# Optimization experiments

Hardware: AMD Instinct MI355X
Metric: run time of the kernel (lower is better)

The kernel has to match this reference:

```python
import jax, jax.numpy as jnp
import numpy as np

N_GRID = 65160   # 181*360 lat-lon grid nodes (= self.size)
N_MESH = 40962   # level-6 icosphere nodes
N_TOT = N_GRID + N_MESH
E = 521280
IN_CH = 96
HID = 256
OUT_CH = 96


def setup_inputs() -> dict:
    key = jax.random.key(0)
    ks = jax.random.split(key, 12)
    inp = {
        'x': jax.random.normal(ks[0], (1, IN_CH, N_MESH), jnp.float32),
        'x_res_grid': jax.random.normal(ks[1], (1, IN_CH, N_GRID), jnp.float32),
        'edge_index': jax.random.randint(ks[2], (2, E), 0, N_TOT, jnp.int64),
        # GCNConv 1 (in_ch -> 256), glorot-ish scale
        'W1': jax.random.normal(ks[3], (IN_CH, HID), jnp.float32) * (2.0 / (IN_CH + HID)) ** 0.5,
        'b1': jnp.zeros((HID,), jnp.float32),
        # GCNConv 2 (256 -> 256)
        'W2': jax.random.normal(ks[4], (HID, HID), jnp.float32) * (2.0 / (HID + HID)) ** 0.5,
        'b2': jnp.zeros((HID,), jnp.float32),
        # Lmodel2: Linear(256,256) -> Linear(256,out_ch), xavier_normal
        'Wl1': jax.random.normal(ks[5], (HID, HID), jnp.float32) * (2.0 / (HID + HID)) ** 0.5,
        'bl1': jnp.zeros((HID,), jnp.float32),
        'Wl2': jax.random.normal(ks[6], (HID, OUT_CH), jnp.float32) * (2.0 / (HID + OUT_CH)) ** 0.5,
        'bl2': jnp.zeros((OUT_CH,), jnp.float32),
    }
    return inp


def _gcn_norm(edge_index, n_nodes):
    # PyG gcn_norm with add_self_loops=True, edge_weight=1
    loop = jnp.arange(n_nodes, dtype=edge_index.dtype)
    src = jnp.concatenate([edge_index[0], loop])
    dst = jnp.concatenate([edge_index[1], loop])
    deg = jnp.zeros((n_nodes,), jnp.float32).at[dst].add(1.0)
    dinv = jnp.where(deg > 0, jax.lax.rsqrt(deg), 0.0)
    norm = dinv[src] * dinv[dst]  # [E+N]
    return src, dst, norm


def _gcn_conv(h, W, b, src, dst, norm):
    # h: [B, N, C] -> [B, N, H]; x' = D^-1/2 (A+I) D^-1/2 (h W) + b
    m = h @ W                                   # [B, N, H]
    msg = m[:, src, :] * norm[None, :, None]    # [B, E+N, H]
    agg = jnp.zeros(m.shape, m.dtype).at[:, dst].add(msg)
    return agg + b


def reference(x, x_res_grid, edge_index, W1, b1, W2, b2, Wl1, bl1, Wl2, bl2):
    nodes = jnp.concatenate([x_res_grid, x], axis=-1)  # [B, C, N]
    h = nodes.transpose(0, 2, 1)                       # [B, N, C]
    n = h.shape[1]
    src, dst, norm = _gcn_norm(edge_index, n)
    h = _gcn_conv(h, W1, b1, src, dst, norm)
    h = jax.nn.gelu(h, approximate=False)              # torch nn.GELU (exact erf)
    h = _gcn_conv(h, W2, b2, src, dst, norm)           # [B, N, 256]
    g = h[:, :N_GRID, :]                               # slice grid nodes
    out = (g @ Wl1 + bl1) @ Wl2 + bl2                  # [B, size, out_ch]
    return out.transpose(0, 2, 1)                      # [B, out_ch, size]
```

## Files before the change

### kernel.cpp

```cpp
#include <hip/hip_runtime.h>
#include <math.h>

#define N_GRID 65160
#define N_MESH 40962
#define N_TOT  106122
#define NE     521280
#define IN_CH  96
#define HID    256
#define OUT_CH 96

typedef __attribute__((ext_vector_type(8))) short bf16x8;
typedef __attribute__((ext_vector_type(4))) float f32x4;

__device__ __forceinline__ unsigned short f2bf(float f) {
  unsigned u = __float_as_uint(f);
  return (unsigned short)((u + 0x7FFFu + ((u >> 16) & 1u)) >> 16);
}
__device__ __forceinline__ float bf2f(unsigned short s) {
  return __uint_as_float(((unsigned)s) << 16);
}
__device__ __forceinline__ float4 ldbf4(const unsigned short* p) {
  ushort4 u = *(const ushort4*)p;
  return make_float4(bf2f(u.x), bf2f(u.y), bf2f(u.z), bf2f(u.w));
}

__global__ void k_concat_transpose(const float* __restrict__ xg, const float* __restrict__ xm,
                                   unsigned short* __restrict__ h) {
  __shared__ float tile[IN_CH][65];
  int base = blockIdx.x * 64;
  int t = threadIdx.x;
#pragma unroll
  for (int it = 0; it < 24; ++it) {
    int lin = t + it * 256;
    int c  = lin >> 6;
    int n0 = lin & 63;
    int n = base + n0;
    float v = 0.f;
    if (n < N_TOT) {
      v = (n < N_GRID) ? xg[(size_t)c * N_GRID + n]
                       : xm[(size_t)c * N_MESH + (n - N_GRID)];
    }
    tile[c][n0] = v;
  }
  __syncthreads();
#pragma unroll
  for (int it = 0; it < 24; ++it) {
    int lin = t + it * 256;
    int c  = lin % 96;
    int n0 = lin / 96;
    int n = base + n0;
    if (n < N_TOT) h[(size_t)n * IN_CH + c] = f2bf(tile[c][n0]);
  }
}

__global__ void k_transpose_out(const float* __restrict__ tb, float* __restrict__ out) {
  __shared__ float tile[IN_CH][65];
  int base = blockIdx.x * 64;
  int t = threadIdx.x;
#pragma unroll
  for (int it = 0; it < 24; ++it) {
    int lin = t + it * 256;
    int c  = lin % 96;
    int n0 = lin / 96;
    int n = base + n0;
    if (n < N_GRID) tile[c][n0] = tb[(size_t)n * 96 + c];
  }
  __syncthreads();
#pragma unroll
  for (int it = 0; it < 24; ++it) {
    int lin = t + it * 256;
    int c  = lin >> 6;
    int n0 = lin & 63;
    int n = base + n0;
    if (n < N_GRID) out[(size_t)c * N_GRID + n] = tile[c][n0];
  }
}

__global__ void k_zeroi(int* __restrict__ p, int n) {
  int i = blockIdx.x * 256 + threadIdx.x;
  if (i < n) p[i] = 0;
}
__global__ void k_seti(int* __restrict__ p, int v) { *p = v; }

__global__ void k_hist(const int* __restrict__ dst, int* __restrict__ deg) {
  int e = blockIdx.x * 256 + threadIdx.x;
  if (e < NE) atomicAdd(&deg[dst[e]], 1);
}

__global__ void k_blocksum(const int* __restrict__ deg, int* __restrict__ bsum, int n) {
  __shared__ int s[256];
  int i = blockIdx.x * 256 + threadIdx.x;
  s[threadIdx.x] = (i < n) ? deg[i] : 0;
  __syncthreads();
  for (int st = 128; st > 0; st >>= 1) {
    if (threadIdx.x < st) s[threadIdx.x] += s[threadIdx.x + st];
    __syncthreads();
  }
  if (threadIdx.x == 0) bsum[blockIdx.x] = s[0];
}

__global__ void k_scanbsum(int* __restrict__ bsum, int nb) {
  __shared__ int s[512];
  int t = threadIdx.x;
  int v = (t < nb) ? bsum[t] : 0;
  s[t] = v;
  __syncthreads();
  for (int off = 1; off < 512; off <<= 1) {
    int x = (t >= off) ? s[t - off] : 0;
    __syncthreads();
    s[t] += x;
    __syncthreads();
  }
  if (t < nb) bsum[t] = s[t] - v;
}

__global__ void k_offsets(const int* __restrict__ deg, const int* __restrict__ bsum,
                          int* __restrict__ off, int* __restrict__ cur, int n) {
  __shared__ int s[256];
  int i = blockIdx.x * 256 + threadIdx.x;
  int v = (i < n) ? deg[i] : 0;
  s[threadIdx.x] = v;
  __syncthreads();
  for (int o = 1; o < 256; o <<= 1) {
    int x = (threadIdx.x >= o) ? s[threadIdx.x - o] : 0;
    __syncthreads();
    s[threadIdx.x] += x;
    __syncthreads();
  }
  if (i < n) {
    int e = bsum[blockIdx.x] + s[threadIdx.x] - v;
    off[i] = e;
    cur[i] = e;
  }
}

__global__ void k_fillcsr(const int* __restrict__ src, const int* __restrict__ dst,
                          int* __restrict__ cur, int* __restrict__ csrc) {
  int e = blockIdx.x * 256 + threadIdx.x;
  if (e < NE) {
    int p = atomicAdd(&cur[dst[e]], 1);
    csrc[p] = src[e];
  }
}

__global__ void k_dinv(const int* __restrict__ deg, float* __restrict__ dinv, int n) {
  int i = blockIdx.x * 256 + threadIdx.x;
  if (i < n) dinv[i] = rsqrtf(1.0f + (float)deg[i]);
}

__global__ void k_gather96(const int* __restrict__ off, const int* __restrict__ csrc,
                           const float* __restrict__ dinv, const unsigned short* __restrict__ h,
                           unsigned short* __restrict__ agg) {
  int i = blockIdx.x * 256 + threadIdx.x;
  if (i >= N_TOT * 24) return;
  int n = i / 24;
  int c4 = (i % 24) << 2;
  float di = dinv[n];
  float4 v = ldbf4(h + (size_t)n * 96 + c4);
  float w0 = di * di;
  float4 acc = make_float4(v.x * w0, v.y * w0, v.z * w0, v.w * w0);
  int e0 = off[n], e1 = off[n + 1];
  int e = e0;
  for (; e + 3 < e1; e += 4) {
    int s0 = csrc[e], s1 = csrc[e + 1], s2 = csrc[e + 2], s3 = csrc[e + 3];
    float wa = dinv[s0] * di, wb = dinv[s1] * di, wc = dinv[s2] * di, wd = dinv[s3] * di;
    float4 u0 = ldbf4(h + (size_t)s0 * 96 + c4);
    float4 u1 = ldbf4(h + (size_t)s1 * 96 + c4);
    float4 u2 = ldbf4(h + (size_t)s2 * 96 + c4);
    float4 u3 = ldbf4(h + (size_t)s3 * 96 + c4);
    acc.x += u0.x * wa + u1.x * wb + u2.x * wc + u3.x * wd;
    acc.y += u0.y * wa + u1.y * wb + u2.y * wc + u3.y * wd;
    acc.z += u0.z * wa + u1.z * wb + u2.z * wc + u3.z * wd;
    acc.w += u0.w * wa + u1.w * wb + u2.w * wc + u3.w * wd;
  }
  for (; e < e1; ++e) {
    int s = csrc[e];
    float w = dinv[s] * di;
    float4 u = ldbf4(h + (size_t)s * 96 + c4);
    acc.x += u.x * w; acc.y += u.y * w; acc.z += u.z * w; acc.w += u.w * w;
  }
  ushort4 o;
  o.x = f2bf(acc.x); o.y = f2bf(acc.y); o.z = f2bf(acc.z); o.w = f2bf(acc.w);
  *(ushort4*)(agg + (size_t)n * 96 + c4) = o;
}

__global__ void k_gather96p(const int* __restrict__ off, const int* __restrict__ csrc,
                            const float* __restrict__ dinv, const float* __restrict__ p,
                            const float* __restrict__ bc, float* __restrict__ tb) {
  int i = blockIdx.x * 256 + threadIdx.x;
  if (i >= N_GRID * 24) return;
  int n = i / 24;
  int c4 = (i % 24) << 2;
  float di = dinv[n];
  float4 v = *(const float4*)(p + (size_t)n * 96 + c4);
  float w0 = di * di;
  float4 acc = make_float4(v.x * w0, v.y * w0, v.z * w0, v.w * w0);
  int e0 = off[n], e1 = off[n + 1];
  int e = e0;
  for (; e + 3 < e1; e += 4) {
    int s0 = csrc[e], s1 = csrc[e + 1], s2 = csrc[e + 2], s3 = csrc[e + 3];
    float wa = dinv[s0] * di, wb = dinv[s1] * di, wc = dinv[s2] * di, wd = dinv[s3] * di;
    float4 u0 = *(const float4*)(p + (size_t)s0 * 96 + c4);
    float4 u1 = *(const float4*)(p + (size_t)s1 * 96 + c4);
    float4 u2 = *(const float4*)(p + (size_t)s2 * 96 + c4);
    float4 u3 = *(const float4*)(p + (size_t)s3 * 96 + c4);
    acc.x += u0.x * wa + u1.x * wb + u2.x * wc + u3.x * wd;
    acc.y += u0.y * wa + u1.y * wb + u2.y * wc + u3.y * wd;
    acc.z += u0.z * wa + u1.z * wb + u2.z * wc + u3.z * wd;
    acc.w += u0.w * wa + u1.w * wb + u2.w * wc + u3.w * wd;
  }
  for (; e < e1; ++e) {
    int s = csrc[e];
    float w = dinv[s] * di;
    float4 u = *(const float4*)(p + (size_t)s * 96 + c4);
    acc.x += u.x * w; acc.y += u.y * w; acc.z += u.z * w; acc.w += u.w * w;
  }
  float4 b = *(const float4*)(bc + c4);
  acc.x += b.x; acc.y += b.y; acc.z += b.z; acc.w += b.w;
  *(float4*)(tb + (size_t)n * 96 + c4) = acc;
}

__global__ __launch_bounds__(256, 2) void k_wgemm96(const float* __restrict__ A, const float* __restrict__ bvec,
                                                    const float* __restrict__ B, float* __restrict__ C,
                                                    int M, int K) {
  __shared__ float As[64][33];
  __shared__ float Bs[64][100];
  int t = threadIdx.x;
  int tx = t & 15, ty = t >> 4;
  int bm = blockIdx.x * 32;
  float acc[2][6] = {};
  for (int kc = 0; kc < K; kc += 64) {
#pragma unroll
    for (int it = 0; it < 2; ++it) {
      int idx = t + it * 256;
      int r = idx >> 4, k4 = (idx & 15) << 2;
      int gr = bm + r;
      float4 v = make_float4(0.f, 0.f, 0.f, 0.f);
      if (gr < M) {
        const float* src = (gr < M - 1) ? (A + (size_t)gr * K + kc + k4) : (bvec + kc + k4);
        v = *(const float4*)src;
      }
      As[k4 + 0][r] = v.x;
      As[k4 + 1][r] = v.y;
      As[k4 + 2][r] = v.z;
      As[k4 + 3][r] = v.w;
    }
#pragma unroll
    for (int it = 0; it < 6; ++it) {
      int idx = t + it * 256;
      int k = idx / 24, j4 = (idx % 24) << 2;
      float4 v = *(const float4*)(B + (size_t)(kc + k) * 96 + j4);
      *(float4*)&Bs[k][j4] = v;
    }
    __syncthreads();
#pragma unroll
    for (int k = 0; k < 64; ++k) {
      float a0 = As[k][ty * 2], a1 = As[k][ty * 2 + 1];
      float w[6];
      *(float2*)&w[0] = *(const float2*)&Bs[k][tx * 6];
      *(float2*)&w[2] = *(const float2*)&Bs[k][tx * 6 + 2];
      *(float2*)&w[4] = *(const float2*)&Bs[k][tx * 6 + 4];
#pragma unroll
      for (int j = 0; j < 6; ++j) { acc[0][j] += a0 * w[j]; acc[1][j] += a1 * w[j]; }
    }
    __syncthreads();
  }
#pragma unroll
  for (int i = 0; i < 2; ++i) {
    int gr = bm + ty * 2 + i;
    if (gr >= M) continue;
    float* row = C + (size_t)gr * 96 + tx * 6;
    row[0] = acc[i][0]; row[1] = acc[i][1]; row[2] = acc[i][2];
    row[3] = acc[i][3]; row[4] = acc[i][4]; row[5] = acc[i][5];
  }
}

__global__ void k_bc_final(const float* __restrict__ r1, const float* __restrict__ r2,
                           const float* __restrict__ bl2, float* __restrict__ bc) {
  int j = threadIdx.x;
  if (j < OUT_CH) bc[j] = r1[j] + r2[j] + bl2[j];
}

__global__ void k_cast_w1t(const float* __restrict__ W1, unsigned short* __restrict__ W1bt) {
  int idx = blockIdx.x * 256 + threadIdx.x;
  if (idx >= 256 * 96) return;
  int n = idx / 96, k = idx % 96;
  W1bt[idx] = f2bf(W1[(size_t)k * 256 + n]);
}
__global__ void k_cast_wct(const float* __restrict__ Wc, unsigned short* __restrict__ Wcbt) {
  int idx = blockIdx.x * 256 + threadIdx.x;
  if (idx >= 96 * 256) return;
  int n = idx / 256, k = idx % 256;
  Wcbt[idx] = f2bf(Wc[(size_t)k * 96 + n]);
}

__global__ __launch_bounds__(256) void k_mgemm1(const unsigned short* __restrict__ A,
                                                const unsigned short* __restrict__ Bt,
                                                const float* __restrict__ bias,
                                                unsigned short* __restrict__ C, int M) {
  __shared__ unsigned short As[64][104];
  __shared__ unsigned short Bs[64][104];
  int t = threadIdx.x;
  int bm = blockIdx.y * 64, bn = blockIdx.x * 64;
#pragma unroll
  for (int it = 0; it < 3; ++it) {
    int idx = t + it * 256;
    int row = idx / 12, g = idx % 12;
    uint4 v = make_uint4(0u, 0u, 0u, 0u);
    if (bm + row < M) v = *(const uint4*)(A + (size_t)(bm + row) * 96 + g * 8);
    *(uint4*)&As[row][g * 8] = v;
  }
#pragma unroll
  for (int it = 0; it < 3; ++it) {
    int idx = t + it * 256;
    int n = idx / 12, g = idx % 12;
    uint4 v = *(const uint4*)(Bt + (size_t)(bn + n) * 96 + g * 8);
    *(uint4*)&Bs[n][g * 8] = v;
  }
  __syncthreads();
  int wave = t >> 6, lane = t & 63;
  int l15 = lane & 15, lhi = lane >> 4;
  f32x4 acc[4];
#pragma unroll
  for (int f = 0; f < 4; ++f) acc[f] = (f32x4){0.f, 0.f, 0.f, 0.f};
  int arow = wave * 16 + l15;
#pragma unroll
  for (int ks = 0; ks < 3; ++ks) {
    bf16x8 a = *(const bf16x8*)&As[arow][ks * 32 + lhi * 8];
#pragma unroll
    for (int f = 0; f < 4; ++f) {
      bf16x8 b = *(const bf16x8*)&Bs[f * 16 + l15][ks * 32 + lhi * 8];
      acc[f] = __builtin_amdgcn_mfma_f32_16x16x32_bf16(a, b, acc[f], 0, 0, 0);
    }
  }
#pragma unroll
  for (int f = 0; f < 4; ++f) {
    int col = bn + f * 16 + l15;
    float bv = bias[col];
#pragma unroll
    for (int r = 0; r < 4; ++r) {
      int row = bm + wave * 16 + lhi * 4 + r;
      if (row < M) {
        float x = acc[f][r] + bv;
        x = 0.5f * x * (1.0f + erff(x * 0.70710678118654752f));
        C[(size_t)row * 256 + col] = f2bf(x);
      }
    }
  }
}

__global__ __launch_bounds__(256) void k_mgemmN96(const unsigned short* __restrict__ A,
                                                  const unsigned short* __restrict__ Bt,
                                                  float* __restrict__ P, int M) {
  __shared__ unsigned short As[64][72];
  __shared__ unsigned short Bs[96][72];
  int t = threadIdx.x;
  int bm = blockIdx.x * 64;
  int wave = t >> 6, lane = t & 63;
  int l15 = lane & 15, lhi = lane >> 4;
  f32x4 acc[6];
#pragma unroll
  for (int f = 0; f < 6; ++f) acc[f] = (f32x4){0.f, 0.f, 0.f, 0.f};
  for (int kc = 0; kc < 4; ++kc) {
#pragma unroll
    for (int it = 0; it < 2; ++it) {
      int idx = t + it * 256;
      int row = idx >> 3, g = idx & 7;
      uint4 v = make_uint4(0u, 0u, 0u, 0u);
      if (bm + row < M) v = *(const uint4*)(A + (size_t)(bm + row) * 256 + kc * 64 + g * 8);
      *(uint4*)&As[row][g * 8] = v;
    }
#pragma unroll
    for (int it = 0; it < 3; ++it) {
      int idx = t + it * 256;
      int n = idx >> 3, g = idx & 7;
      uint4 v = *(const uint4*)(Bt + (size_t)n * 256 + kc * 64 + g * 8);
      *(uint4*)&Bs[n][g * 8] = v;
    }
    __syncthreads();
#pragma unroll
    for (int ks = 0; ks < 2; ++ks) {
      bf16x8 a = *(const bf16x8*)&As[wave * 16 + l15][ks * 32 + lhi * 8];
#pragma unroll
      for (int f = 0; f < 6; ++f) {
        bf16x8 b = *(const bf16x8*)&Bs[f * 16 + l15][ks * 32 + lhi * 8];
        acc[f] = __builtin_amdgcn_mfma_f32_16x16x32_bf16(a, b, acc[f], 0, 0, 0);
      }
    }
    __syncthreads();
  }
#pragma unroll
  for (int f = 0; f < 6; ++f) {
    int col = f * 16 + l15;
#pragma unroll
    for (int r = 0; r < 4; ++r) {
      int row = bm + wave * 16 + lhi * 4 + r;
      if (row < M) P[(size_t)row * 96 + col] = acc[f][r];
    }
  }
}

extern "C" void kernel_launch(void* const* d_in, const int* in_sizes, int n_in,
                              void* d_out, int out_size, void* d_ws, size_t ws_size,
                              hipStream_t stream) {
  const float* xm  = (const float*)d_in[0];
  const float* xg  = (const float*)d_in[1];
  const int*   ei  = (const int*)d_in[2];
  const float* W1  = (const float*)d_in[3];
  const float* b1  = (const float*)d_in[4];
  const float* W2  = (const float*)d_in[5];
  const float* b2  = (const float*)d_in[6];
  const float* Wl1 = (const float*)d_in[7];
  const float* bl1 = (const float*)d_in[8];
  const float* Wl2 = (const float*)d_in[9];
  const float* bl2 = (const float*)d_in[10];
  float* out = (float*)d_out;

  float* W0 = (float*)d_ws;
  const size_t MB = (size_t)N_GRID * 256;
  int*   deg  = (int*)(W0 + MB);
  int*   off  = deg + N_TOT;
  int*   cur  = off + N_TOT + 1;
  int*   bsum = cur + N_TOT;
  int*   csrc = bsum + 512;
  float* dinv = (float*)(csrc + NE);
  size_t p1off = ((size_t)(dinv + N_TOT - W0) + 3) & ~(size_t)3;
  float* P1 = W0 + p1off;
  float* P2 = P1 + 257 * 96;
  float* bc = P2 + 257 * 96;
  size_t wboff = ((size_t)(bc + 96 - W0) + 3) & ~(size_t)3;
  unsigned short* W1bt = (unsigned short*)(W0 + wboff);
  unsigned short* Wcbt = W1bt + 256 * 96;
  size_t RH = wboff + 24576 / 2 * 2;
  RH = (RH + 24576 + 3) & ~(size_t)3;
  unsigned short* hb   = (unsigned short*)(W0 + RH);
  unsigned short* h1b  = (unsigned short*)(W0 + RH);
  unsigned short* agg1b = (unsigned short*)W0;
  float* p  = W0;
  float* tb = W0 + (size_t)N_TOT * 96;

  const int* esrc = ei;
  const int* edst = ei + NE;
  dim3 b256(256);
  const int NB_N = (N_TOT + 255) / 256;

  k_concat_transpose<<<dim3((N_TOT + 63) / 64), b256, 0, stream>>>(xg, xm, hb);

  k_zeroi<<<dim3(NB_N), b256, 0, stream>>>(deg, N_TOT);
  k_hist<<<dim3((NE + 255) / 256), b256, 0, stream>>>(edst, deg);
  k_blocksum<<<dim3(NB_N), b256, 0, stream>>>(deg, bsum, N_TOT);
  k_scanbsum<<<dim3(1), dim3(512), 0, stream>>>(bsum, NB_N);
  k_offsets<<<dim3(NB_N), b256, 0, stream>>>(deg, bsum, off, cur, N_TOT);
  k_seti<<<dim3(1), dim3(1), 0, stream>>>(off + N_TOT, NE);
  k_fillcsr<<<dim3((NE + 255) / 256), b256, 0, stream>>>(esrc, edst, cur, csrc);
  k_dinv<<<dim3(NB_N), b256, 0, stream>>>(deg, dinv, N_TOT);
  k_cast_w1t<<<dim3(96), b256, 0, stream>>>(W1, W1bt);

  k_gather96<<<dim3((N_TOT * 24 + 255) / 256), b256, 0, stream>>>(off, csrc, dinv, hb, agg1b);

  k_mgemm1<<<dim3(4, (N_TOT + 63) / 64), b256, 0, stream>>>(agg1b, W1bt, b1, h1b, N_TOT);

  k_wgemm96<<<dim3(9), b256, 0, stream>>>(Wl1, bl1, Wl2, P1, 257, HID);
  k_wgemm96<<<dim3(9), b256, 0, stream>>>(W2, b2, P1, P2, 257, HID);
  k_bc_final<<<dim3(1), dim3(96), 0, stream>>>(P1 + 256 * 96, P2 + 256 * 96, bl2, bc);
  k_cast_wct<<<dim3(96), b256, 0, stream>>>(P2, Wcbt);

  k_mgemmN96<<<dim3((N_TOT + 63) / 64), b256, 0, stream>>>(h1b, Wcbt, p, N_TOT);

  k_gather96p<<<dim3((N_GRID * 24 + 255) / 256), b256, 0, stream>>>(off, csrc, dinv, p, bc, tb);

  k_transpose_out<<<dim3((N_GRID + 63) / 64), b256, 0, stream>>>(tb, out);
}
```

Measured before the change: 263.5 us.

## Fuse layer-1 gather, GEMM+GELU and the 96-column GEMM into one kernel

Replaces three launches (gather96, mgemm1, mgemmN96) with a single kernel per 64-row tile. The kernel gathers normalized neighbour features into LDS, runs the 96→256 MFMA GEMM with GELU into an LDS tile, then multiplies by the folded 256→96 weight. This removes the global write and read of the N_TOT×96 aggregate and the N_TOT×256 hidden activations. In exchange, each thread now runs six gather tasks in sequence instead of one, so fewer independent memory requests are in flight to hide gather latency. Weight operands are also read straight from global/L2 rather than staged in LDS.

```diff
diff --git a/kernel.cpp b/kernel.cpp
--- a/kernel.cpp
+++ b/kernel.cpp
@@ -146,42 +146,6 @@
 __global__ void k_dinv(const int* __restrict__ deg, float* __restrict__ dinv, int n) {
   int i = blockIdx.x * 256 + threadIdx.x;
   if (i < n) dinv[i] = rsqrtf(1.0f + (float)deg[i]);
-}
-
-__global__ void k_gather96(const int* __restrict__ off, const int* __restrict__ csrc,
-                           const float* __restrict__ dinv, const unsigned short* __restrict__ h,
-                           unsigned short* __restrict__ agg) {
-  int i = blockIdx.x * 256 + threadIdx.x;
-  if (i >= N_TOT * 24) return;
-  int n = i / 24;
-  int c4 = (i % 24) << 2;
-  float di = dinv[n];
-  float4 v = ldbf4(h + (size_t)n * 96 + c4);
-  float w0 = di * di;
-  float4 acc = make_float4(v.x * w0, v.y * w0, v.z * w0, v.w * w0);
-  int e0 = off[n], e1 = off[n + 1];
-  int e = e0;
-  for (; e + 3 < e1; e += 4) {
-    int s0 = csrc[e], s1 = csrc[e + 1], s2 = csrc[e + 2], s3 = csrc[e + 3];
-    float wa = dinv[s0] * di, wb = dinv[s1] * di, wc = dinv[s2] * di, wd = dinv[s3] * di;
-    float4 u0 = ldbf4(h + (size_t)s0 * 96 + c4);
-    float4 u1 = ldbf4(h + (size_t)s1 * 96 + c4);
-    float4 u2 = ldbf4(h + (size_t)s2 * 96 + c4);
-    float4 u3 = ldbf4(h + (size_t)s3 * 96 + c4);
-    acc.x += u0.x * wa + u1.x * wb + u2.x * wc + u3.x * wd;
-    acc.y += u0.y * wa + u1.y * wb + u2.y * wc + u3.y * wd;
-    acc.z += u0.z * wa + u1.z * wb + u2.z * wc + u3.z * wd;
-    acc.w += u0.w * wa + u1.w * wb + u2.w * wc + u3.w * wd;
-  }
-  for (; e < e1; ++e) {
-    int s = csrc[e];
-    float w = dinv[s] * di;
-    float4 u = ldbf4(h + (size_t)s * 96 + c4);
-    acc.x += u.x * w; acc.y += u.y * w; acc.z += u.z * w; acc.w += u.w * w;
-  }
-  ushort4 o;
-  o.x = f2bf(acc.x); o.y = f2bf(acc.y); o.z = f2bf(acc.z); o.w = f2bf(acc.w);
-  *(ushort4*)(agg + (size_t)n * 96 + c4) = o;
 }
 
 __global__ void k_gather96p(const int* __restrict__ off, const int* __restrict__ csrc,
@@ -294,108 +258,110 @@
   Wcbt[idx] = f2bf(Wc[(size_t)k * 96 + n]);
 }
 
-__global__ __launch_bounds__(256) void k_mgemm1(const unsigned short* __restrict__ A,
-                                                const unsigned short* __restrict__ Bt,
-                                                const float* __restrict__ bias,
-                                                unsigned short* __restrict__ C, int M) {
+__global__ __launch_bounds__(256) void k_fused(const int* __restrict__ off, const int* __restrict__ csrc,
+                                               const float* __restrict__ dinv,
+                                               const unsigned short* __restrict__ hb,
+                                               const unsigned short* __restrict__ W1bt,
+                                               const float* __restrict__ b1,
+                                               const unsigned short* __restrict__ Wcbt,
+                                               float* __restrict__ P, int M) {
   __shared__ unsigned short As[64][104];
-  __shared__ unsigned short Bs[64][104];
+  __shared__ unsigned short Hs[64][264];
   int t = threadIdx.x;
-  int bm = blockIdx.y * 64, bn = blockIdx.x * 64;
-#pragma unroll
-  for (int it = 0; it < 3; ++it) {
-    int idx = t + it * 256;
-    int row = idx / 12, g = idx % 12;
-    uint4 v = make_uint4(0u, 0u, 0u, 0u);
-    if (bm + row < M) v = *(const uint4*)(A + (size_t)(bm + row) * 96 + g * 8);
-    *(uint4*)&As[row][g * 8] = v;
-  }
-#pragma unroll
-  for (int it = 0; it < 3; ++it) {
-    int idx = t + it * 256;
-    int n = idx / 12, g = idx % 12;
-    uint4 v = *(const uint4*)(Bt + (size_t)(bn + n) * 96 + g * 8);
-    *(uint4*)&Bs[n][g * 8] = v;
-  }
-  __syncthreads();
   int wave = t >> 6, lane = t & 63;
   int l15 = lane & 15, lhi = lane >> 4;
-  f32x4 acc[4];
-#pragma unroll
-  for (int f = 0; f < 4; ++f) acc[f] = (f32x4){0.f, 0.f, 0.f, 0.f};
-  int arow = wave * 16 + l15;
-#pragma unroll
-  for (int ks = 0; ks < 3; ++ks) {
-    bf16x8 a = *(const bf16x8*)&As[arow][ks * 32 + lhi * 8];
-#pragma unroll
-    for (int f = 0; f < 4; ++f) {
-      bf16x8 b = *(const bf16x8*)&Bs[f * 16 + l15][ks * 32 + lhi * 8];
-      acc[f] = __builtin_amdgcn_mfma_f32_16x16x32_bf16(a, b, acc[f], 0, 0, 0);
-    }
-  }
-#pragma unroll
-  for (int f = 0; f < 4; ++f) {
-    int col = bn + f * 16 + l15;
-    float bv = bias[col];
-#pragma unroll
-    for (int r = 0; r < 4; ++r) {
-      int row = bm + wave * 16 + lhi * 4 + r;
-      if (row < M) {
-        float x = acc[f][r] + bv;
+  int bm = blockIdx.x * 64;
+
+#pragma unroll
+  for (int it = 0; it < 6; ++it) {
+    int task = lane + it * 64;
+    int r = task / 24;
+    int c4 = (task % 24) << 2;
+    int row = wave * 16 + r;
+    int n = bm + row;
+    float4 acc = make_float4(0.f, 0.f, 0.f, 0.f);
+    if (n < M) {
+      float di = dinv[n];
+      float4 v = ldbf4(hb + (size_t)n * 96 + c4);
+      float w0 = di * di;
+      acc = make_float4(v.x * w0, v.y * w0, v.z * w0, v.w * w0);
+      int e0 = off[n], e1 = off[n + 1];
+      int e = e0;
+      for (; e + 3 < e1; e += 4) {
+        int s0 = csrc[e], s1 = csrc[e + 1], s2 = csrc[e + 2], s3 = csrc[e + 3];
+        float wa = dinv[s0] * di, wb = dinv[s1] * di, wc = dinv[s2] * di, wd = dinv[s3] * di;
+        float4 u0 = ldbf4(hb + (size_t)s0 * 96 + c4);
+        float4 u1 = ldbf4(hb + (size_t)s1 * 96 + c4);
+        float4 u2 = ldbf4(hb + (size_t)s2 * 96 + c4);
+        float4 u3 = ldbf4(hb + (size_t)s3 * 96 + c4);
+        acc.x += u0.x * wa + u1.x * wb + u2.x * wc + u3.x * wd;
+        acc.y += u0.y * wa + u1.y * wb + u2.y * wc + u3.y * wd;
+        acc.z += u0.z * wa + u1.z * wb + u2.z * wc + u3.z * wd;
+        acc.w += u0.w * wa + u1.w * wb + u2.w * wc + u3.w * wd;
+      }
+      for (; e < e1; ++e) {
+        int s = csrc[e];
+        float w = dinv[s] * di;
+        float4 u = ldbf4(hb + (size_t)s * 96 + c4);
+        acc.x += u.x * w; acc.y += u.y * w; acc.z += u.z * w; acc.w += u.w * w;
+      }
+    }
+    ushort4 o;
+    o.x = f2bf(acc.x); o.y = f2bf(acc.y); o.z = f2bf(acc.z); o.w = f2bf(acc.w);
+    *(ushort4*)&As[row][c4] = o;
+  }
+  __syncthreads();
+
+  {
+    f32x4 acc1[16];
+#pragma unroll
+    for (int f = 0; f < 16; ++f) acc1[f] = (f32x4){0.f, 0.f, 0.f, 0.f};
+    int arow = wave * 16 + l15;
+#pragma unroll
+    for (int ks = 0; ks < 3; ++ks) {
+      bf16x8 a = *(const bf16x8*)&As[arow][ks * 32 + lhi * 8];
+#pragma unroll
+      for (int f = 0; f < 16; ++f) {
+        bf16x8 b = *(const bf16x8*)(W1bt + (size_t)(f * 16 + l15) * 96 + ks * 32 + lhi * 8);
+        acc1[f] = __builtin_amdgcn_mfma_f32_16x16x32_bf16(a, b, acc1[f], 0, 0, 0);
+      }
+    }
+#pragma unroll
+    for (int f = 0; f < 16; ++f) {
+      int col = f * 16 + l15;
+      float bv = b1[col];
+#pragma unroll
+      for (int r = 0; r < 4; ++r) {
+        float x = acc1[f][r] + bv;
         x = 0.5f * x * (1.0f + erff(x * 0.70710678118654752f));
-        C[(size_t)row * 256 + col] = f2bf(x);
-      }
-    }
-  }
-}
-
-__global__ __launch_bounds__(256) void k_mgemmN96(const unsigned short* __restrict__ A,
-                                                  const unsigned short* __restrict__ Bt,
-                                                  float* __restrict__ P, int M) {
-  __shared__ unsigned short As[64][72];
-  __shared__ unsigned short Bs[96][72];
-  int t = threadIdx.x;
-  int bm = blockIdx.x * 64;
-  int wave = t >> 6, lane = t & 63;
-  int l15 = lane & 15, lhi = lane >> 4;
-  f32x4 acc[6];
-#pragma unroll
-  for (int f = 0; f < 6; ++f) acc[f] = (f32x4){0.f, 0.f, 0.f, 0.f};
-  for (int kc = 0; kc < 4; ++kc) {
-#pragma unroll
-    for (int it = 0; it < 2; ++it) {
-      int idx = t + it * 256;
-      int row = idx >> 3, g = idx & 7;
-      uint4 v = make_uint4(0u, 0u, 0u, 0u);
-      if (bm + row < M) v = *(const uint4*)(A + (size_t)(bm + row) * 256 + kc * 64 + g * 8);
-      *(uint4*)&As[row][g * 8] = v;
-    }
-#pragma unroll
-    for (int it = 0; it < 3; ++it) {
-      int idx = t + it * 256;
-      int n = idx >> 3, g = idx & 7;
-      uint4 v = *(const uint4*)(Bt + (size_t)n * 256 + kc * 64 + g * 8);
-      *(uint4*)&Bs[n][g * 8] = v;
-    }
-    __syncthreads();
-#pragma unroll
-    for (int ks = 0; ks < 2; ++ks) {
-      bf16x8 a = *(const bf16x8*)&As[wave * 16 + l15][ks * 32 + lhi * 8];
+        Hs[wave * 16 + lhi * 4 + r][col] = f2bf(x);
+      }
+    }
+  }
+  __syncthreads();
+
+  {
+    f32x4 acc2[6];
+#pragma unroll
+    for (int f = 0; f < 6; ++f) acc2[f] = (f32x4){0.f, 0.f, 0.f, 0.f};
+    int hrow = wave * 16 + l15;
+#pragma unroll
+    for (int ks = 0; ks < 8; ++ks) {
+      bf16x8 a = *(const bf16x8*)&Hs[hrow][ks * 32 + lhi * 8];
 #pragma unroll
       for (int f = 0; f < 6; ++f) {
-        bf16x8 b = *(const bf16x8*)&Bs[f * 16 + l15][ks * 32 + lhi * 8];
-        acc[f] = __builtin_amdgcn_mfma_f32_16x16x32_bf16(a, b, acc[f], 0, 0, 0);
-      }
-    }
-    __syncthreads();
-  }
-#pragma unroll
-  for (int f = 0; f < 6; ++f) {
-    int col = f * 16 + l15;
-#pragma unroll
-    for (int r = 0; r < 4; ++r) {
-      int row = bm + wave * 16 + lhi * 4 + r;
-      if (row < M) P[(size_t)row * 96 + col] = acc[f][r];
+        bf16x8 b = *(const bf16x8*)(Wcbt + (size_t)(f * 16 + l15) * 256 + ks * 32 + lhi * 8);
+        acc2[f] = __builtin_amdgcn_mfma_f32_16x16x32_bf16(a, b, acc2[f], 0, 0, 0);
+      }
+    }
+#pragma unroll
+    for (int f = 0; f < 6; ++f) {
+      int col = f * 16 + l15;
+#pragma unroll
+      for (int r = 0; r < 4; ++r) {
+        int row = bm + wave * 16 + lhi * 4 + r;
+        if (row < M) P[(size_t)row * 96 + col] = acc2[f][r];
+      }
     }
   }
 }
@@ -431,11 +397,8 @@
   size_t wboff = ((size_t)(bc + 96 - W0) + 3) & ~(size_t)3;
   unsigned short* W1bt = (unsigned short*)(W0 + wboff);
   unsigned short* Wcbt = W1bt + 256 * 96;
-  size_t RH = wboff + 24576 / 2 * 2;
-  RH = (RH + 24576 + 3) & ~(size_t)3;
-  unsigned short* hb   = (unsigned short*)(W0 + RH);
-  unsigned short* h1b  = (unsigned short*)(W0 + RH);
-  unsigned short* agg1b = (unsigned short*)W0;
+  size_t RH = (wboff + 24576 + 3) & ~(size_t)3;
+  unsigned short* hb = (unsigned short*)(W0 + RH);
   float* p  = W0;
   float* tb = W0 + (size_t)N_TOT * 96;
 
@@ -455,17 +418,12 @@
   k_fillcsr<<<dim3((NE + 255) / 256), b256, 0, stream>>>(esrc, edst, cur, csrc);
   k_dinv<<<dim3(NB_N), b256, 0, stream>>>(deg, dinv, N_TOT);
   k_cast_w1t<<<dim3(96), b256, 0, stream>>>(W1, W1bt);
-
-  k_gather96<<<dim3((N_TOT * 24 + 255) / 256), b256, 0, stream>>>(off, csrc, dinv, hb, agg1b);
-
-  k_mgemm1<<<dim3(4, (N_TOT + 63) / 64), b256, 0, stream>>>(agg1b, W1bt, b1, h1b, N_TOT);
-
   k_wgemm96<<<dim3(9), b256, 0, stream>>>(Wl1, bl1, Wl2, P1, 257, HID);
   k_wgemm96<<<dim3(9), b256, 0, stream>>>(W2, b2, P1, P2, 257, HID);
   k_bc_final<<<dim3(1), dim3(96), 0, stream>>>(P1 + 256 * 96, P2 + 256 * 96, bl2, bc);
   k_cast_wct<<<dim3(96), b256, 0, stream>>>(P2, Wcbt);
 
-  k_mgemmN96<<<dim3((N_TOT + 63) / 64), b256, 0, stream>>>(h1b, Wcbt, p, N_TOT);
+  k_fused<<<dim3((N_TOT + 63) / 64), b256, 0, stream>>>(off, csrc, dinv, hb, W1bt, b1, Wcbt, p, N_TOT);
 
   k_gather96p<<<dim3((N_GRID * 24 + 255) / 256), b256, 0, stream>>>(off, csrc, dinv, p, bc, tb);
 
```

Result: slower. 336.0 us (+27.5%).
